# Kernel tuning notes

Measured on AMD Instinct MI355X. Metric: run time of the kernel, lower is better.

Reference implementation:

```python
import jax, jax.numpy as jnp
import numpy as np

NUM_HEADS = 8
NUM_LEVELS = 4
NUM_POINTS = 8
EMBED = 256
SPATIAL_SHAPES = ((92, 160), (46, 80), (23, 40), (12, 20))


def _bilinear_sample(vl, gx, gy, H, W):
    # vl: [N, d, H*W]; gx, gy: [N, Q, P], grid coords in [-1, 1]
    # matches F.grid_sample(mode='bilinear', padding_mode='zeros', align_corners=False)
    x = (gx + 1.0) * (W * 0.5) - 0.5
    y = (gy + 1.0) * (H * 0.5) - 0.5
    x0 = jnp.floor(x)
    y0 = jnp.floor(y)
    wx = x - x0
    wy = y - y0
    x0i = x0.astype(jnp.int32)
    y0i = y0.astype(jnp.int32)
    N, Q, P = gx.shape
    d = vl.shape[1]

    def gather(xi, yi):
        valid = ((xi >= 0) & (xi < W) & (yi >= 0) & (yi < H)).astype(vl.dtype)
        idx = jnp.clip(yi, 0, H - 1) * W + jnp.clip(xi, 0, W - 1)  # [N, Q, P]
        flat = jnp.broadcast_to(idx.reshape(N, 1, Q * P), (N, d, Q * P))
        got = jnp.take_along_axis(vl, flat, axis=2).reshape(N, d, Q, P)
        return got * valid[:, None]

    return (gather(x0i, y0i) * ((1 - wx) * (1 - wy))[:, None]
            + gather(x0i + 1, y0i) * (wx * (1 - wy))[:, None]
            + gather(x0i, y0i + 1) * ((1 - wx) * wy)[:, None]
            + gather(x0i + 1, y0i + 1) * (wx * wy)[:, None])


def _forward(query, value, reference_points, spatial_shapes,
             W_off, b_off, W_attn, b_attn, W_val, b_val, W_out, b_out):
    shapes = np.asarray(spatial_shapes)  # static per-level (H, W)
    bs, Q, C = query.shape
    H, Lv, P = NUM_HEADS, NUM_LEVELS, NUM_POINTS
    d = C // H
    # value projection, split into heads: [bs*H, d, Ltot]
    v = value @ W_val + b_val
    v = v.reshape(bs, -1, H, d).transpose(0, 2, 3, 1).reshape(bs * H, d, -1)
    # sampling offsets [bs, Q, H, Lv, P, 2]
    off = (query @ W_off + b_off).reshape(bs, Q, H, Lv, P, 2)
    # attention weights, softmax over Lv*P
    aw = jax.nn.softmax((query @ W_attn + b_attn).reshape(bs, Q, H, Lv * P), axis=-1)
    aw = aw.reshape(bs, Q, H, Lv, P).transpose(0, 2, 1, 3, 4).reshape(bs * H, Q, Lv, P)
    # normalize offsets by level (W, H)
    norm = jnp.asarray([[w_, h_] for h_, w_ in shapes], dtype=query.dtype)  # [Lv, 2]
    loc = reference_points[:, :, None, :, None, :] + off / norm[None, None, None, :, None, :]
    grids = (2.0 * loc - 1.0).transpose(0, 2, 1, 3, 4, 5).reshape(bs * H, Q, Lv, P, 2)
    out = jnp.zeros((bs * H, d, Q), dtype=query.dtype)
    start = 0
    for lvl in range(Lv):
        H_l, W_l = int(shapes[lvl, 0]), int(shapes[lvl, 1])
        vl = v[:, :, start:start + H_l * W_l]
        g = grids[:, :, lvl]  # [bs*H, Q, P, 2]
        s = _bilinear_sample(vl, g[..., 0], g[..., 1], H_l, W_l)  # [bs*H, d, Q, P]
        out = out + jnp.einsum('ndqp,nqp->ndq', s, aw[:, :, lvl])
        start += H_l * W_l
    out = out.reshape(bs, H, d, Q).transpose(0, 3, 1, 2).reshape(bs, Q, C)
    return out @ W_out + b_out


def setup_inputs() -> dict:
    key = jax.random.key(0)
    ks = jax.random.split(key, 9)
    bs, Q = 6, 4096  # 6 cameras x (64x64 BEV queries)
    Ltot = sum(h * w for h, w in SPATIAL_SHAPES)  # 19560
    HLP2 = NUM_HEADS * NUM_LEVELS * NUM_POINTS * 2  # 512
    HLP = NUM_HEADS * NUM_LEVELS * NUM_POINTS  # 256
    s = 0.02
    return {
        "query": jax.random.normal(ks[0], (bs, Q, EMBED), jnp.float32),
        "value": jax.random.normal(ks[1], (bs, Ltot, EMBED), jnp.float32),
        "reference_points": jax.random.uniform(ks[2], (bs, Q, NUM_LEVELS, 2), jnp.float32),
        "spatial_shapes": jnp.asarray(SPATIAL_SHAPES, jnp.int32),
        "W_off": s * jax.random.normal(ks[3], (EMBED, HLP2), jnp.float32),
        "b_off": s * jax.random.normal(ks[4], (HLP2,), jnp.float32),
        "W_attn": s * jax.random.normal(ks[5], (EMBED, HLP), jnp.float32),
        "b_attn": s * jax.random.normal(ks[6], (HLP,), jnp.float32),
        "W_val": s * jax.random.normal(ks[7], (EMBED, EMBED), jnp.float32),
        "b_val": jnp.zeros((EMBED,), jnp.float32),
        "W_out": s * jax.random.normal(ks[8], (EMBED, EMBED), jnp.float32),
        "b_out": jnp.zeros((EMBED,), jnp.float32),
    }


def reference(query, value, reference_points, spatial_shapes,
              W_off, b_off, W_attn, b_attn, W_val, b_val, W_out, b_out):
    return _forward(query, value, reference_points, spatial_shapes,
                    W_off, b_off, W_attn, b_attn, W_val, b_val, W_out, b_out)
```

## Files before the change

### kernel.cpp

```cpp
#include <hip/hip_runtime.h>
#include <stdint.h>

#define BS 6
#define NQ 4096
#define NH 8
#define EMB 256
#define LTOT 19560
#define ROWS_V 117360
#define ROWS_VP 117376
#define ROWS_Q 24576

typedef __attribute__((ext_vector_type(8))) short bf16x8;
typedef __attribute__((ext_vector_type(4))) float floatx4;
typedef __attribute__((ext_vector_type(8))) unsigned short ushort8v;

__device__ __forceinline__ ushort f2bf(float f) {
    union { float f; uint32_t i; } c; c.f = f;
    uint32_t r = c.i + 0x7FFFu + ((c.i >> 16) & 1u);
    return (ushort)(r >> 16);
}
__device__ __forceinline__ float bflo(uint32_t u) {
    union { uint32_t i; float f; } c; c.i = u << 16; return c.f;
}
__device__ __forceinline__ float bfhi(uint32_t u) {
    union { uint32_t i; float f; } c; c.i = u & 0xFFFF0000u; return c.f;
}

__device__ __forceinline__ void gll16(const ushort* g, ushort* l) {
    __builtin_amdgcn_global_load_lds(
        (const __attribute__((address_space(1))) void*)g,
        (__attribute__((address_space(3))) void*)l, 16, 0, 0);
}

__global__ __launch_bounds__(256) void cast_bf16(
    const float* __restrict__ in, ushort* __restrict__ out, int n)
{
    int i = (blockIdx.x * 256 + threadIdx.x) * 8;
    if (i >= n) return;
    float4 f0 = *(const float4*)(in + i);
    float4 f1 = *(const float4*)(in + i + 4);
    ushort8v r;
    r[0] = f2bf(f0.x); r[1] = f2bf(f0.y); r[2] = f2bf(f0.z); r[3] = f2bf(f0.w);
    r[4] = f2bf(f1.x); r[5] = f2bf(f1.y); r[6] = f2bf(f1.z); r[7] = f2bf(f1.w);
    *(ushort8v*)(out + i) = r;
}

__global__ __launch_bounds__(256) void cast_t(
    const float* __restrict__ W, ushort* __restrict__ Wt, int N_)
{
    int id = blockIdx.x * 256 + threadIdx.x;
    if (id >= 256 * N_) return;
    int n = id >> 8;
    int k = id & 255;
    Wt[id] = f2bf(W[(size_t)k * N_ + n]);
}

__global__ __launch_bounds__(768) void bias_concat(
    const float* __restrict__ b_off, const float* __restrict__ b_attn,
    float* __restrict__ bcat)
{
    int i = threadIdx.x;
    bcat[i] = (i < 512) ? b_off[i] : b_attn[i - 512];
}

__global__ __launch_bounds__(512) void vgemm(
    const float* __restrict__ A,
    const ushort* __restrict__ Bt,
    const float* __restrict__ bias,
    ushort* __restrict__ C)
{
    constexpr int K = 256, N = 256, M = ROWS_V;
    __shared__ ushort As[128 * 32];
    __shared__ ushort Bs[256 * 32];

    const int t = threadIdx.x;
    const int w = t >> 6;
    const int lane = t & 63;
    const int bm = blockIdx.x * 128;
    const int wm = (w >> 2) * 64;
    const int wn = (w & 3) * 64;

    const int arow = t >> 2;
    const int acol = (t & 3) * 8;
    const bool rowok = (bm + arow) < M;
    const float* Ap = A + (size_t)(bm + arow) * K + acol;
    ushort* Asw = &As[arow * 32 + acol];

    const int srow = lane >> 2;
    const int scol = (lane & 3) * 8;
    const ushort* Bg0 = Bt + (size_t)(w * 32 + srow) * K + scol;
    const ushort* Bg1 = Bt + (size_t)(w * 32 + 16 + srow) * K + scol;
    ushort* Bl0 = &Bs[(w * 32) * 32];
    ushort* Bl1 = &Bs[(w * 32 + 16) * 32];

    const ushort* apt = &As[(wm + (lane & 15)) * 32 + (lane >> 4) * 8];
    const ushort* bpt = &Bs[(wn + (lane & 15)) * 32 + (lane >> 4) * 8];

    floatx4 acc[4][4] = {};

    for (int kt = 0; kt < K; kt += 32) {
        float4 f0, f1;
        if (rowok) {
            f0 = *(const float4*)(Ap + kt);
            f1 = *(const float4*)(Ap + kt + 4);
        } else {
            f0 = make_float4(0.f, 0.f, 0.f, 0.f);
            f1 = f0;
        }
        __syncthreads();
        gll16(Bg0 + kt, Bl0);
        gll16(Bg1 + kt, Bl1);
        ushort8v u;
        u[0] = f2bf(f0.x); u[1] = f2bf(f0.y); u[2] = f2bf(f0.z); u[3] = f2bf(f0.w);
        u[4] = f2bf(f1.x); u[5] = f2bf(f1.y); u[6] = f2bf(f1.z); u[7] = f2bf(f1.w);
        *(ushort8v*)Asw = u;
        __syncthreads();

        bf16x8 a[4], b[4];
        #pragma unroll
        for (int i = 0; i < 4; ++i) {
            a[i] = *(const bf16x8*)(apt + i * 16 * 32);
            b[i] = *(const bf16x8*)(bpt + i * 16 * 32);
        }
        #pragma unroll
        for (int i = 0; i < 4; ++i)
            #pragma unroll
            for (int j = 0; j < 4; ++j)
                acc[i][j] = __builtin_amdgcn_mfma_f32_16x16x32_bf16(
                    a[i], b[j], acc[i][j], 0, 0, 0);
    }

    const int crow = (lane >> 4) * 4;
    const int ccol = lane & 15;
    #pragma unroll
    for (int j = 0; j < 4; ++j) {
        int gcol = wn + j * 16 + ccol;
        float bv = bias[gcol];
        #pragma unroll
        for (int i = 0; i < 4; ++i) {
            #pragma unroll
            for (int r = 0; r < 4; ++r) {
                int grow = bm + wm + i * 16 + crow + r;
                if (grow < M)
                    C[(size_t)grow * N + gcol] = f2bf(acc[i][j][r] + bv);
            }
        }
    }
}

__global__ __launch_bounds__(256) void gemm_bt(
    const ushort* __restrict__ A,
    const ushort* __restrict__ Bt,
    const float* __restrict__ bias,
    float* __restrict__ C, int M, int N)
{
    constexpr int K = 256;
    __shared__ ushort As[128 * 32];
    __shared__ ushort Bs[128 * 32];

    const int t = threadIdx.x;
    const int w = t >> 6;
    const int lane = t & 63;
    const int bm = blockIdx.x * 128;
    const int bn = blockIdx.y * 128;
    const int wm = (w >> 1) * 64;
    const int wn = (w & 1) * 64;

    floatx4 acc[4][4] = {};

    const int srow = lane >> 2;
    const int scol = (lane & 3) * 8;
    const ushort* Ag0 = A + (size_t)(bm + (w * 2 + 0) * 16 + srow) * K + scol;
    const ushort* Ag1 = A + (size_t)(bm + (w * 2 + 1) * 16 + srow) * K + scol;
    const ushort* Bg0 = Bt + (size_t)(bn + (w * 2 + 0) * 16 + srow) * K + scol;
    const ushort* Bg1 = Bt + (size_t)(bn + (w * 2 + 1) * 16 + srow) * K + scol;
    ushort* Al0 = &As[(w * 2 + 0) * 512];
    ushort* Al1 = &As[(w * 2 + 1) * 512];
    ushort* Bl0 = &Bs[(w * 2 + 0) * 512];
    ushort* Bl1 = &Bs[(w * 2 + 1) * 512];

    const ushort* apt = &As[(wm + (lane & 15)) * 32 + (lane >> 4) * 8];
    const ushort* bpt = &Bs[(wn + (lane & 15)) * 32 + (lane >> 4) * 8];

    for (int kt = 0; kt < K; kt += 32) {
        __syncthreads();
        gll16(Ag0 + kt, Al0);
        gll16(Ag1 + kt, Al1);
        gll16(Bg0 + kt, Bl0);
        gll16(Bg1 + kt, Bl1);
        __syncthreads();

        bf16x8 a[4], b[4];
        #pragma unroll
        for (int i = 0; i < 4; ++i) {
            a[i] = *(const bf16x8*)(apt + i * 16 * 32);
            b[i] = *(const bf16x8*)(bpt + i * 16 * 32);
        }
        #pragma unroll
        for (int i = 0; i < 4; ++i)
            #pragma unroll
            for (int j = 0; j < 4; ++j)
                acc[i][j] = __builtin_amdgcn_mfma_f32_16x16x32_bf16(
                    a[i], b[j], acc[i][j], 0, 0, 0);
    }

    const int crow = (lane >> 4) * 4;
    const int ccol = lane & 15;
    #pragma unroll
    for (int j = 0; j < 4; ++j) {
        int gcol = bn + wn + j * 16 + ccol;
        float bv = bias[gcol];
        #pragma unroll
        for (int i = 0; i < 4; ++i) {
            #pragma unroll
            for (int r = 0; r < 4; ++r) {
                int grow = bm + wm + i * 16 + crow + r;
                if (grow < M)
                    C[(size_t)grow * N + gcol] = acc[i][j][r] + bv;
            }
        }
    }
}

__global__ __launch_bounds__(256) void sampler4(
    const ushort* __restrict__ v,
    const float* __restrict__ qp,
    const float* __restrict__ ref,
    ushort* __restrict__ agg)
{
    const int tid = threadIdx.x;
    const int g = blockIdx.x * 64 + (tid >> 2);
    const int st = tid & 3;
    const int h = g & 7;
    const int bq = g >> 3;
    const int b = bq >> 12;

    float o[16];
    {
        const float* offp = qp + (size_t)bq * 768 + h * 64 + st * 16;
        #pragma unroll
        for (int i = 0; i < 4; ++i)
            *(float4*)&o[i * 4] = *(const float4*)(offp + i * 4);
    }
    float a8[8];
    {
        const float* lp = qp + (size_t)bq * 768 + 512 + h * 32 + st * 8;
        *(float4*)&a8[0] = *(const float4*)(lp);
        *(float4*)&a8[4] = *(const float4*)(lp + 4);
        float m = a8[0];
        #pragma unroll
        for (int i = 1; i < 8; ++i) m = fmaxf(m, a8[i]);
        m = fmaxf(m, __shfl_xor(m, 1, 4));
        m = fmaxf(m, __shfl_xor(m, 2, 4));
        float s = 0.f;
        #pragma unroll
        for (int i = 0; i < 8; ++i) { a8[i] = __expf(a8[i] - m); s += a8[i]; }
        s += __shfl_xor(s, 1, 4);
        s += __shfl_xor(s, 2, 4);
        float inv = 1.f / s;
        #pragma unroll
        for (int i = 0; i < 8; ++i) a8[i] *= inv;
    }
    float rf[8];
    *(float4*)&rf[0] = *(const float4*)(ref + (size_t)bq * 8);
    *(float4*)&rf[4] = *(const float4*)(ref + (size_t)bq * 8 + 4);

    const ushort* vb = v + (size_t)b * LTOT * EMB + h * 32 + st * 8;

    const int LW[4] = {160, 80, 40, 20};
    const int LH[4] = {92, 46, 23, 12};
    const int LS[4] = {0, 14720, 18400, 19320};

    float acc[8] = {0.f, 0.f, 0.f, 0.f, 0.f, 0.f, 0.f, 0.f};

    #pragma unroll
    for (int k = 0; k < 32; ++k) {
        const int l = k >> 3;
        const int W = LW[l], Hh = LH[l], S = LS[l];
        const int idx = k & 7;
        float awk = __shfl(a8[idx], k >> 3, 4);
        float ox  = __shfl(o[2 * idx], k >> 3, 4);
        float oy  = __shfl(o[2 * idx + 1], k >> 3, 4);

        float px = fmaf(rf[2 * l], (float)W, ox) - 0.5f;
        float py = fmaf(rf[2 * l + 1], (float)Hh, oy) - 0.5f;
        float x0f = floorf(px), y0f = floorf(py);
        float wx = px - x0f, wy = py - y0f;
        int x0 = (int)x0f, y0 = (int)y0f;
        int x1 = x0 + 1, y1 = y0 + 1;

        float vx0 = (x0 >= 0 && x0 < W) ? 1.f : 0.f;
        float vx1 = (x1 >= 0 && x1 < W) ? 1.f : 0.f;
        float vy0 = (y0 >= 0 && y0 < Hh) ? 1.f : 0.f;
        float vy1 = (y1 >= 0 && y1 < Hh) ? 1.f : 0.f;
        int cx0 = min(max(x0, 0), W - 1);
        int cx1 = min(max(x1, 0), W - 1);
        int cy0 = min(max(y0, 0), Hh - 1);
        int cy1 = min(max(y1, 0), Hh - 1);

        float w00 = (1.f - wx) * (1.f - wy) * vx0 * vy0 * awk;
        float w10 = wx * (1.f - wy) * vx1 * vy0 * awk;
        float w01 = (1.f - wx) * wy * vx0 * vy1 * awk;
        float w11 = wx * wy * vx1 * vy1 * awk;

        uint4 c00 = *(const uint4*)(vb + (size_t)(S + cy0 * W + cx0) * EMB);
        uint4 c10 = *(const uint4*)(vb + (size_t)(S + cy0 * W + cx1) * EMB);
        uint4 c01 = *(const uint4*)(vb + (size_t)(S + cy1 * W + cx0) * EMB);
        uint4 c11 = *(const uint4*)(vb + (size_t)(S + cy1 * W + cx1) * EMB);

        #define ACC8(w_, c_) \
            acc[0] = fmaf(w_, bflo(c_.x), acc[0]); acc[1] = fmaf(w_, bfhi(c_.x), acc[1]); \
            acc[2] = fmaf(w_, bflo(c_.y), acc[2]); acc[3] = fmaf(w_, bfhi(c_.y), acc[3]); \
            acc[4] = fmaf(w_, bflo(c_.z), acc[4]); acc[5] = fmaf(w_, bfhi(c_.z), acc[5]); \
            acc[6] = fmaf(w_, bflo(c_.w), acc[6]); acc[7] = fmaf(w_, bfhi(c_.w), acc[7]);
        ACC8(w00, c00);
        ACC8(w10, c10);
        ACC8(w01, c01);
        ACC8(w11, c11);
        #undef ACC8
    }

    ushort8v r;
    #pragma unroll
    for (int i = 0; i < 8; ++i) r[i] = f2bf(acc[i]);
    *(ushort8v*)(agg + (size_t)bq * 256 + h * 32 + st * 8) = r;
}

extern "C" void kernel_launch(void* const* d_in, const int* in_sizes, int n_in,
                              void* d_out, int out_size, void* d_ws, size_t ws_size,
                              hipStream_t stream) {
    const float* query  = (const float*)d_in[0];
    const float* value  = (const float*)d_in[1];
    const float* refpts = (const float*)d_in[2];
    const float* W_off  = (const float*)d_in[4];
    const float* b_off  = (const float*)d_in[5];
    const float* W_attn = (const float*)d_in[6];
    const float* b_attn = (const float*)d_in[7];
    const float* W_val  = (const float*)d_in[8];
    const float* b_val  = (const float*)d_in[9];
    const float* W_out  = (const float*)d_in[10];
    const float* b_out  = (const float*)d_in[11];
    float* out = (float*)d_out;

    char* ws = (char*)d_ws;
    ushort* v_bf   = (ushort*)(ws);
    ushort* q_bf   = (ushort*)(ws + 60096512ull);
    float*  qp     = (float*) (ws + 72679424ull);
    ushort* agg_bf = (ushort*)(ws + 148176896ull);
    ushort* Wvt    = (ushort*)(ws + 160759808ull);
    ushort* Wq     = (ushort*)(ws + 160890880ull);
    ushort* Wot    = (ushort*)(ws + 161284096ull);
    float*  bcat   = (float*) (ws + 161415168ull);

    cast_t<<<(256 * 256) / 256, 256, 0, stream>>>(W_val, Wvt, 256);
    cast_t<<<(256 * 512) / 256, 256, 0, stream>>>(W_off, Wq, 512);
    cast_t<<<(256 * 256) / 256, 256, 0, stream>>>(W_attn, Wq + 512 * 256, 256);
    cast_t<<<(256 * 256) / 256, 256, 0, stream>>>(W_out, Wot, 256);
    bias_concat<<<1, 768, 0, stream>>>(b_off, b_attn, bcat);
    cast_bf16<<<(ROWS_Q * EMB / 8) / 256, 256, 0, stream>>>(
        query, q_bf, ROWS_Q * EMB);

    vgemm<<<ROWS_VP / 128, 512, 0, stream>>>(value, Wvt, b_val, v_bf);

    gemm_bt<<<dim3(ROWS_Q / 128, 6), 256, 0, stream>>>(
        q_bf, Wq, bcat, qp, ROWS_Q, 768);

    sampler4<<<(ROWS_Q * NH) / 64, 256, 0, stream>>>(
        v_bf, qp, refpts, agg_bf);

    gemm_bt<<<dim3(ROWS_Q / 128, 2), 256, 0, stream>>>(
        agg_bf, Wot, b_out, out, ROWS_Q, 256);
}
```

Measured before the change: 421.5 us.

## Store values as fp16, use fma_mix and swizzle-broadcast level-parallel sampling

The value projection GEMM now writes fp16 instead of bf16, and the sampler accumulates with v_fma_mix_f32, which reads the packed halves directly instead of unpacking bf16 with shifts and masks. Each of the four lanes in a group now computes the corner weights and addresses for its own level, and ds_swizzle broadcasts them, replacing per-point shuffles and redundant coordinate math. Addresses use 32-bit byte offsets and launch bounds request 6 waves per SIMD. Switching to fp16 narrows the exponent range of the stored values, and the sampler's final output cast is unchanged, so a downstream consumer may still read agg as bf16.

```diff
diff --git a/kernel.cpp b/kernel.cpp
--- a/kernel.cpp
+++ b/kernel.cpp
@@ -1,4 +1,5 @@
 #include <hip/hip_runtime.h>
+#include <hip/hip_fp16.h>
 #include <stdint.h>
 
 #define BS 6
@@ -19,17 +20,34 @@
     uint32_t r = c.i + 0x7FFFu + ((c.i >> 16) & 1u);
     return (ushort)(r >> 16);
 }
-__device__ __forceinline__ float bflo(uint32_t u) {
-    union { uint32_t i; float f; } c; c.i = u << 16; return c.f;
-}
-__device__ __forceinline__ float bfhi(uint32_t u) {
-    union { uint32_t i; float f; } c; c.i = u & 0xFFFF0000u; return c.f;
+__device__ __forceinline__ ushort f2h(float f) {
+    __half h = __float2half(f);
+    union { __half h; ushort u; } c; c.h = h; return c.u;
 }
 
 __device__ __forceinline__ void gll16(const ushort* g, ushort* l) {
     __builtin_amdgcn_global_load_lds(
         (const __attribute__((address_space(1))) void*)g,
         (__attribute__((address_space(3))) void*)l, 16, 0, 0);
+}
+
+template<int L>
+__device__ __forceinline__ float bcastf(float x) {
+    return __int_as_float(
+        __builtin_amdgcn_ds_swizzle(__float_as_int(x), 0x1C | (L << 5)));
+}
+template<int L>
+__device__ __forceinline__ uint32_t bcastu(uint32_t x) {
+    return (uint32_t)__builtin_amdgcn_ds_swizzle((int)x, 0x1C | (L << 5));
+}
+
+__device__ __forceinline__ void fmx_lo(float& acc, float w, uint32_t u) {
+    asm("v_fma_mix_f32 %0, %1, %2, %0 op_sel:[0,0,0] op_sel_hi:[0,1,0]"
+        : "+v"(acc) : "v"(w), "v"(u));
+}
+__device__ __forceinline__ void fmx_hi(float& acc, float w, uint32_t u) {
+    asm("v_fma_mix_f32 %0, %1, %2, %0 op_sel:[0,1,0] op_sel_hi:[0,1,0]"
+        : "+v"(acc) : "v"(w), "v"(u));
 }
 
 __global__ __launch_bounds__(256) void cast_bf16(
@@ -142,7 +160,7 @@
             for (int r = 0; r < 4; ++r) {
                 int grow = bm + wm + i * 16 + crow + r;
                 if (grow < M)
-                    C[(size_t)grow * N + gcol] = f2bf(acc[i][j][r] + bv);
+                    C[(size_t)grow * N + gcol] = f2h(acc[i][j][r] + bv);
             }
         }
     }
@@ -222,7 +240,7 @@
     }
 }
 
-__global__ __launch_bounds__(256) void sampler4(
+__global__ __launch_bounds__(256, 6) void sampler4(
     const ushort* __restrict__ v,
     const float* __restrict__ qp,
     const float* __restrict__ ref,
@@ -233,15 +251,28 @@
     const int st = tid & 3;
     const int h = g & 7;
     const int bq = g >> 3;
-    const int b = bq >> 12;
-
-    float o[16];
+    const int b = blockIdx.x >> 9;
+
+    const int Wl = 160 >> st;
+    const int Hl = (st == 3) ? 12 : (92 >> st);
+    const int Sl = (st == 0) ? 0 : (st == 1) ? 14720 : (st == 2) ? 18400 : 19320;
+
+    float px[8], py[8];
     {
         const float* offp = qp + (size_t)bq * 768 + h * 64 + st * 16;
+        float o[16];
         #pragma unroll
         for (int i = 0; i < 4; ++i)
             *(float4*)&o[i * 4] = *(const float4*)(offp + i * 4);
-    }
+        float2 rf = *(const float2*)(ref + (size_t)bq * 8 + st * 2);
+        const float fW = (float)Wl, fH = (float)Hl;
+        #pragma unroll
+        for (int i = 0; i < 8; ++i) {
+            px[i] = fmaf(rf.x, fW, o[2 * i]) - 0.5f;
+            py[i] = fmaf(rf.y, fH, o[2 * i + 1]) - 0.5f;
+        }
+    }
+
     float a8[8];
     {
         const float* lp = qp + (size_t)bq * 768 + 512 + h * 32 + st * 8;
@@ -261,63 +292,63 @@
         #pragma unroll
         for (int i = 0; i < 8; ++i) a8[i] *= inv;
     }
-    float rf[8];
-    *(float4*)&rf[0] = *(const float4*)(ref + (size_t)bq * 8);
-    *(float4*)&rf[4] = *(const float4*)(ref + (size_t)bq * 8 + 4);
-
-    const ushort* vb = v + (size_t)b * LTOT * EMB + h * 32 + st * 8;
-
-    const int LW[4] = {160, 80, 40, 20};
-    const int LH[4] = {92, 46, 23, 12};
-    const int LS[4] = {0, 14720, 18400, 19320};
+
+    const char* vb = (const char*)(v + (size_t)b * (LTOT * EMB));
+    const uint32_t coffB = (uint32_t)(h * 64 + st * 16);
 
     float acc[8] = {0.f, 0.f, 0.f, 0.f, 0.f, 0.f, 0.f, 0.f};
 
     #pragma unroll
-    for (int k = 0; k < 32; ++k) {
-        const int l = k >> 3;
-        const int W = LW[l], Hh = LH[l], S = LS[l];
-        const int idx = k & 7;
-        float awk = __shfl(a8[idx], k >> 3, 4);
-        float ox  = __shfl(o[2 * idx], k >> 3, 4);
-        float oy  = __shfl(o[2 * idx + 1], k >> 3, 4);
-
-        float px = fmaf(rf[2 * l], (float)W, ox) - 0.5f;
-        float py = fmaf(rf[2 * l + 1], (float)Hh, oy) - 0.5f;
-        float x0f = floorf(px), y0f = floorf(py);
-        float wx = px - x0f, wy = py - y0f;
+    for (int idx = 0; idx < 8; ++idx) {
+        float px_ = px[idx], py_ = py[idx];
+        float x0f = floorf(px_), y0f = floorf(py_);
+        float wx = px_ - x0f, wy = py_ - y0f;
         int x0 = (int)x0f, y0 = (int)y0f;
         int x1 = x0 + 1, y1 = y0 + 1;
-
-        float vx0 = (x0 >= 0 && x0 < W) ? 1.f : 0.f;
-        float vx1 = (x1 >= 0 && x1 < W) ? 1.f : 0.f;
-        float vy0 = (y0 >= 0 && y0 < Hh) ? 1.f : 0.f;
-        float vy1 = (y1 >= 0 && y1 < Hh) ? 1.f : 0.f;
-        int cx0 = min(max(x0, 0), W - 1);
-        int cx1 = min(max(x1, 0), W - 1);
-        int cy0 = min(max(y0, 0), Hh - 1);
-        int cy1 = min(max(y1, 0), Hh - 1);
-
-        float w00 = (1.f - wx) * (1.f - wy) * vx0 * vy0 * awk;
-        float w10 = wx * (1.f - wy) * vx1 * vy0 * awk;
-        float w01 = (1.f - wx) * wy * vx0 * vy1 * awk;
-        float w11 = wx * wy * vx1 * vy1 * awk;
-
-        uint4 c00 = *(const uint4*)(vb + (size_t)(S + cy0 * W + cx0) * EMB);
-        uint4 c10 = *(const uint4*)(vb + (size_t)(S + cy0 * W + cx1) * EMB);
-        uint4 c01 = *(const uint4*)(vb + (size_t)(S + cy1 * W + cx0) * EMB);
-        uint4 c11 = *(const uint4*)(vb + (size_t)(S + cy1 * W + cx1) * EMB);
-
-        #define ACC8(w_, c_) \
-            acc[0] = fmaf(w_, bflo(c_.x), acc[0]); acc[1] = fmaf(w_, bfhi(c_.x), acc[1]); \
-            acc[2] = fmaf(w_, bflo(c_.y), acc[2]); acc[3] = fmaf(w_, bfhi(c_.y), acc[3]); \
-            acc[4] = fmaf(w_, bflo(c_.z), acc[4]); acc[5] = fmaf(w_, bfhi(c_.z), acc[5]); \
-            acc[6] = fmaf(w_, bflo(c_.w), acc[6]); acc[7] = fmaf(w_, bfhi(c_.w), acc[7]);
-        ACC8(w00, c00);
-        ACC8(w10, c10);
-        ACC8(w01, c01);
-        ACC8(w11, c11);
-        #undef ACC8
+        float vx0 = ((uint32_t)x0 < (uint32_t)Wl) ? 1.f : 0.f;
+        float vx1 = ((uint32_t)x1 < (uint32_t)Wl) ? 1.f : 0.f;
+        float vy0 = ((uint32_t)y0 < (uint32_t)Hl) ? 1.f : 0.f;
+        float vy1 = ((uint32_t)y1 < (uint32_t)Hl) ? 1.f : 0.f;
+        int cx0 = min(max(x0, 0), Wl - 1);
+        int cx1 = min(max(x1, 0), Wl - 1);
+        int cy0 = min(max(y0, 0), Hl - 1);
+        int cy1 = min(max(y1, 0), Hl - 1);
+        float aw = a8[idx];
+        float omx = 1.f - wx, omy = 1.f - wy;
+        float omya = omy * aw, wya = wy * aw;
+        float w00 = omx * omya * (vx0 * vy0);
+        float w10 = wx  * omya * (vx1 * vy0);
+        float w01 = omx * wya  * (vx0 * vy1);
+        float w11 = wx  * wya  * (vx1 * vy1);
+        int r0 = Sl + cy0 * Wl;
+        int r1 = Sl + cy1 * Wl;
+        uint32_t e00 = (uint32_t)(r0 + cx0) << 9;
+        uint32_t e10 = (uint32_t)(r0 + cx1) << 9;
+        uint32_t e01 = (uint32_t)(r1 + cx0) << 9;
+        uint32_t e11 = (uint32_t)(r1 + cx1) << 9;
+
+        #define ACCMIX(w_, c_) \
+            fmx_lo(acc[0], w_, c_.x); fmx_hi(acc[1], w_, c_.x); \
+            fmx_lo(acc[2], w_, c_.y); fmx_hi(acc[3], w_, c_.y); \
+            fmx_lo(acc[4], w_, c_.z); fmx_hi(acc[5], w_, c_.z); \
+            fmx_lo(acc[6], w_, c_.w); fmx_hi(acc[7], w_, c_.w);
+        #define DO_LEVEL(L) { \
+            float W00 = bcastf<L>(w00), W10 = bcastf<L>(w10); \
+            float W01 = bcastf<L>(w01), W11 = bcastf<L>(w11); \
+            uint32_t E00 = bcastu<L>(e00), E10 = bcastu<L>(e10); \
+            uint32_t E01 = bcastu<L>(e01), E11 = bcastu<L>(e11); \
+            uint4 c00 = *(const uint4*)(vb + (E00 + coffB)); \
+            uint4 c10 = *(const uint4*)(vb + (E10 + coffB)); \
+            uint4 c01 = *(const uint4*)(vb + (E01 + coffB)); \
+            uint4 c11 = *(const uint4*)(vb + (E11 + coffB)); \
+            ACCMIX(W00, c00); ACCMIX(W10, c10); \
+            ACCMIX(W01, c01); ACCMIX(W11, c11); }
+        DO_LEVEL(0)
+        DO_LEVEL(1)
+        DO_LEVEL(2)
+        DO_LEVEL(3)
+        #undef DO_LEVEL
+        #undef ACCMIX
     }
 
     ushort8v r;
```

Result: slower. 500.4 us (+18.7%).
